# Kernel tuning notes

Hardware: AMD Instinct MI355X
Metric: run time of the kernel (lower is better)

Reference implementation:

```python
import jax, jax.numpy as jnp
import numpy as np

T, B, I = 512, 64, 768
H, L = 768, 2


def setup_inputs() -> dict:
    key = jax.random.key(0)
    ks = jax.random.split(key, 8)
    s = 1.0 / np.sqrt(H)
    return {
        "event_seq": jax.random.normal(ks[0], (T, B, I), jnp.float32),
        "h0": jax.random.normal(ks[1], (L, B, H), jnp.float32),
        "c0": jax.random.normal(ks[2], (L, B, H), jnp.float32),
        "W_ih": jax.random.uniform(ks[3], (L, 4 * H, I), jnp.float32, -s, s),
        "W_hh": jax.random.uniform(ks[4], (L, 4 * H, H), jnp.float32, -s, s),
        "b_ih": jax.random.uniform(ks[5], (L, 4 * H), jnp.float32, -s, s),
        "b_hh": jax.random.uniform(ks[6], (L, 4 * H), jnp.float32, -s, s),
        "length": jax.random.randint(ks[7], (B,), 1, T + 1, jnp.int32),
    }


def reference(event_seq, h0, c0, W_ih, W_hh, b_ih, b_hh, length):
    # event_seq: [T, B, I]; h0/c0: [L, B, H]; W_ih/W_hh: [L, 4H, *]
    ts = jnp.arange(event_seq.shape[0])

    def step(carry, xt_t):
        h, c = carry                      # [L, B, H] each
        x_t, t = xt_t
        mask = (t < length).astype(x_t.dtype)[:, None]  # [B, 1]
        x = x_t
        hs, cs = [], []
        for l in range(L):
            gates = x @ W_ih[l].T + b_ih[l] + h[l] @ W_hh[l].T + b_hh[l]
            i_g, f_g, g_g, o_g = jnp.split(gates, 4, axis=-1)  # torch LSTMCell order
            c_new = jax.nn.sigmoid(f_g) * c[l] + jax.nn.sigmoid(i_g) * jnp.tanh(g_g)
            h_new = jax.nn.sigmoid(o_g) * jnp.tanh(c_new)
            h_new = mask * h_new + (1.0 - mask) * h[l]
            c_new = mask * c_new + (1.0 - mask) * c[l]
            hs.append(h_new)
            cs.append(c_new)
            x = h_new  # dropout=0 -> identity between layers
        h = jnp.stack(hs)
        c = jnp.stack(cs)
        return (h, c), h

    (h_f, c_f), out = jax.lax.scan(step, (h0, c0), (event_seq, ts))
    # out: [T, L, B, H] -> [T, B, L, H] (matches torch.stack(..., dim=2))
    out = out.transpose(0, 2, 1, 3)
    return out, h_f, c_f
```

## Files before the change

### kernel.cpp

```cpp
#include <hip/hip_runtime.h>

typedef unsigned short u16;
typedef unsigned int u32;
typedef unsigned long long u64;
typedef __attribute__((ext_vector_type(8))) short short8;
typedef __attribute__((ext_vector_type(4))) float f32x4;

#define T_STEPS 512
#define HF_OFF 50331648UL
#define SLOT 49152

#define BCAT_OFF 18874368UL
#define HB0_OFF  18898944UL
#define HB1_OFF  (HB0_OFF + 32UL*98304UL)
#define FLG_OFF  (HB1_OFF + 4UL*98304UL)

__device__ __forceinline__ u16 f2bf(float f) {
  union { float f; unsigned u; } v; v.f = f;
  unsigned r = (v.u + 0x7FFFu + ((v.u >> 16) & 1u)) >> 16;
  return (u16)r;
}

__device__ __forceinline__ short8 pack8(float4 f0, float4 f1) {
  short8 v;
  v[0]=(short)f2bf(f0.x); v[1]=(short)f2bf(f0.y); v[2]=(short)f2bf(f0.z); v[3]=(short)f2bf(f0.w);
  v[4]=(short)f2bf(f1.x); v[5]=(short)f2bf(f1.y); v[6]=(short)f2bf(f1.z); v[7]=(short)f2bf(f1.w);
  return v;
}

__device__ __forceinline__ float sigm(float x) { return 1.0f / (1.0f + __expf(-x)); }
__device__ __forceinline__ float tanh_f(float x) { return 1.0f - 2.0f / (__expf(2.0f * x) + 1.0f); }

__device__ __forceinline__ short8 load_sc_b128(const void* p) {
  short8 r;
  asm volatile("global_load_dwordx4 %0, %1, off sc0 sc1" : "=&v"(r) : "v"((u64)p));
  return r;
}
__device__ __forceinline__ u32 load_sc_b32(const u32* p) {
  u32 r;
  asm volatile("global_load_dword %0, %1, off sc0 sc1\n\ts_waitcnt vmcnt(0)"
               : "=&v"(r) : "v"((u64)p) : "memory");
  return r;
}
__device__ __forceinline__ void store_sc_b32(u32* p, u32 v) {
  asm volatile("global_store_dword %0, %1, off sc0 sc1" :: "v"((u64)p), "v"(v) : "memory");
}

__device__ __forceinline__ void poll1(const u32* base, int own) {
  const int ln = threadIdx.x & 63;
  for (;;) {
    u32 f = load_sc_b32(base + ln);
    if (ln == own) f = 1u;
    if (__all(f != 0)) break;
    __builtin_amdgcn_s_sleep(1);
  }
}

__device__ __forceinline__ void stage_u16(u16* dstL, const u16* srcRow, int row, int uu) {
  short8 hv[6];
#pragma unroll
  for (int i = 0; i < 6; ++i) {
    int unit = uu + i * 16;
    int kel = (unit * 8) ^ ((row & 7) << 3);
    hv[i] = load_sc_b128(srcRow + kel);
  }
  __builtin_amdgcn_sched_barrier(0);
  asm volatile("s_waitcnt vmcnt(0)" ::: "memory");
  __builtin_amdgcn_sched_barrier(0);
#pragma unroll
  for (int i = 0; i < 6; ++i) {
    int unit = uu + i * 16;
    *(short8*)((char*)dstL + row * 1536 + unit * 16) = hv[i];
  }
}

__device__ __forceinline__ void stage_xf(u16* dstL, const float* srcRow, int row, int uu) {
#pragma unroll
  for (int i = 0; i < 6; ++i) {
    int unit = uu + i * 16;
    int kel = (unit * 8) ^ ((row & 7) << 3);
    float4 f0 = *(const float4*)(srcRow + kel);
    float4 f1 = *(const float4*)(srcRow + kel + 4);
    *(short8*)((char*)dstL + row * 1536 + unit * 16) = pack8(f0, f1);
  }
}

__global__ void prep_weights(const float* __restrict__ Wih, const float* __restrict__ Whh,
                             u16* __restrict__ Wr) {
  int idx = blockIdx.x * blockDim.x + threadIdx.x;
  if (idx >= 2 * 3072 * 192) return;
  int r = idx / 192;
  int kc = (idx - r * 192) * 8;
  int l = r / 3072;
  int rr = r - l * 3072;
  int j = rr >> 2, g = rr & 3;
  int srow = l * 3072 + g * 768 + j;
  const float* src = (kc < 768) ? (Wih + (size_t)srow * 768 + kc)
                                : (Whh + (size_t)srow * 768 + (kc - 768));
  float4 f0 = *(const float4*)src;
  float4 f1 = *(const float4*)(src + 4);
  *(short8*)(Wr + (size_t)r * 1536 + kc) = pack8(f0, f1);
}

__global__ void prep_misc(const float* __restrict__ h0, const float* __restrict__ bih,
                          const float* __restrict__ bhh, u16* __restrict__ hb0,
                          u16* __restrict__ hb1, float* __restrict__ bcat,
                          u32* __restrict__ flags) {
  int idx = blockIdx.x * blockDim.x + threadIdx.x;
  if (idx < 131584) {
    flags[idx] = (((idx >> 7) % 514) == 0) ? 1u : 0u;
  } else if (idx < 131584 + 98304) {
    int r = idx - 131584;
    int l = r / 49152, o = r - l * 49152;
    u16 v = f2bf(h0[r]);
    if (l == 0) hb0[o] = v; else hb1[o] = v;
  } else if (idx < 131584 + 98304 + 6144) {
    int q = idx - (131584 + 98304);
    int l = q / 3072, rr = q - l * 3072;
    int j = rr >> 2, g = rr & 3;
    int s = l * 3072 + g * 768 + j;
    bcat[q] = bih[s] + bhh[s];
  }
}

__global__ void __launch_bounds__(512, 1)
lstm_dataflow(const float* __restrict__ x, const float* __restrict__ h0,
              const float* __restrict__ c0, const int* __restrict__ len,
              const u16* __restrict__ Wr, const float* __restrict__ bcat,
              u16* __restrict__ hb0, u16* __restrict__ hb1,
              u32* __restrict__ flags, float* __restrict__ out) {
  __shared__ u16 lAh[32 * 768];
  __shared__ u16 lAx[32 * 768];
  __shared__ float pP[48 * 32 * 4];
  __shared__ u16 lH[32 * 12];

  const int tid = threadIdx.x;
  const int wv = tid >> 6;
  const int ln = tid & 63;
  const int ks = wv & 3;
  const int rt = wv >> 2;
  const int wg = blockIdx.x;
  const int layer = wg >> 7;
  const int rg = (wg >> 6) & 1;
  const int cg = wg & 63;
  const int n0 = cg * 48;
  const int row = tid >> 4;
  const int uu = tid & 15;
  const int arow = rt * 16 + (ln & 15);

  short8 Wx[3][6], Wh[3][6];
  {
    const u16* wbase = Wr + (size_t)(layer * 3072 + n0) * 1536;
#pragma unroll
    for (int ct = 0; ct < 3; ++ct)
#pragma unroll
      for (int kst = 0; kst < 6; ++kst) {
        int col = ct * 16 + (ln & 15);
        int k = ks * 192 + kst * 32 + ((ln >> 4) << 3);
        Wx[ct][kst] = *(const short8*)(wbase + (size_t)col * 1536 + k);
        Wh[ct][kst] = *(const short8*)(wbase + (size_t)col * 1536 + 768 + k);
      }
  }
  float bc[3] = {0.f, 0.f, 0.f};
  if (ks == 0) {
#pragma unroll
    for (int ct = 0; ct < 3; ++ct)
      bc[ct] = bcat[layer * 3072 + n0 + ct * 16 + (ln & 15)];
  }
  const int cellb = tid / 12, cellj = tid - (tid / 12) * 12;
  float cReg = 0.f, hKeep = 0.f; int lenB = 0;
  if (tid < 384) {
    int b = rg * 32 + cellb, j = cg * 12 + cellj;
    cReg = c0[(size_t)(layer * 64 + b) * 768 + j];
    hKeep = h0[(size_t)(layer * 64 + b) * 768 + j];
    lenB = len[b];
  }

  f32x4 acc_x[3];
  auto run_xmfma = [&]() {
#pragma unroll
    for (int ct = 0; ct < 3; ++ct)
      acc_x[ct] = (ks == 0) ? (f32x4){bc[ct], bc[ct], bc[ct], bc[ct]}
                            : (f32x4){0.f, 0.f, 0.f, 0.f};
#pragma unroll
    for (int kst = 0; kst < 6; ++kst) {
      int kel = ks * 192 + kst * 32 + ((ln >> 4) << 3);
      short8 a = *(const short8*)((const char*)lAx + arow * 1536 + ((kel * 2) ^ ((arow & 7) << 4)));
#pragma unroll
      for (int ct = 0; ct < 3; ++ct)
        acc_x[ct] = __builtin_amdgcn_mfma_f32_16x16x32_bf16(a, Wx[ct][kst], acc_x[ct], 0, 0, 0);
    }
  };
  auto stage_x = [&](int u) {
    if (layer == 0) {
      stage_xf(lAx, x + ((size_t)u * 64 + rg * 32 + row) * 768, row, uu);
    } else {
      poll1(flags + ((size_t)(0 * 514 + (u + 1)) * 2 + rg) * 64, -1);
      stage_u16(lAx, hb0 + (size_t)((u + 1) & 31) * SLOT + (size_t)(rg * 32 + row) * 768, row, uu);
    }
  };

  stage_x(0);
  __syncthreads();
  run_xmfma();
  __syncthreads();

  for (int t = 0; t < T_STEPS; ++t) {
    if (t < T_STEPS - 1) stage_x(t + 1);

    poll1(flags + ((size_t)(layer * 514 + t) * 2 + rg) * 64, cg);
    {
      const u16* hp = (layer == 0) ? hb0 + (size_t)(t & 31) * SLOT
                                   : hb1 + (size_t)(t & 3) * SLOT;
      stage_u16(lAh, hp + (size_t)(rg * 32 + row) * 768, row, uu);
    }
    __syncthreads();

    f32x4 acc[3];
#pragma unroll
    for (int ct = 0; ct < 3; ++ct) acc[ct] = acc_x[ct];
#pragma unroll
    for (int kst = 0; kst < 6; ++kst) {
      int kel = ks * 192 + kst * 32 + ((ln >> 4) << 3);
      short8 a = *(const short8*)((const char*)lAh + arow * 1536 + ((kel * 2) ^ ((arow & 7) << 4)));
#pragma unroll
      for (int ct = 0; ct < 3; ++ct)
        acc[ct] = __builtin_amdgcn_mfma_f32_16x16x32_bf16(a, Wh[ct][kst], acc[ct], 0, 0, 0);
    }

#pragma unroll
    for (int ct = 0; ct < 3; ++ct) {
      int col = ct * 16 + (ln & 15);
      int kwp = ks ^ (col & 3);
#pragma unroll
      for (int i = 0; i < 4; ++i) {
        int bloc = rt * 16 + ((ln >> 4) << 2) + i;
        pP[col * 128 + ((bloc ^ (col & 7)) << 2) + kwp] = acc[ct][i];
      }
    }
    __syncthreads();

    if (tid < 384) {
      float g4[4];
#pragma unroll
      for (int g = 0; g < 4; ++g) {
        int col = cellj * 4 + g;
        f32x4 v = *(const f32x4*)&pP[col * 128 + ((cellb ^ (col & 7)) << 2)];
        g4[g] = (v[0] + v[1]) + (v[2] + v[3]);
      }
      float cn = sigm(g4[1]) * cReg + sigm(g4[0]) * tanh_f(g4[2]);
      float hn = sigm(g4[3]) * tanh_f(cn);
      const bool act = t < lenB;
      float hm = act ? hn : hKeep;
      float cm = act ? cn : cReg;
      hKeep = hm; cReg = cm;
      const int bglob = rg * 32 + cellb, jglob = cg * 12 + cellj;
      lH[cellb * 12 + cellj] = f2bf(hm);
      out[((size_t)(t * 64 + bglob) * 2 + layer) * 768 + jglob] = hm;
    }
    __syncthreads();

    if (wv == 7) {
      u16* hout = (layer == 0) ? hb0 + (size_t)((t + 1) & 31) * SLOT
                               : hb1 + (size_t)((t + 1) & 3) * SLOT;
      const u32* lH32 = (const u32*)lH;
#pragma unroll
      for (int it = 0; it < 3; ++it) {
        int idx = ln + it * 64;
        int r = idx / 6, w = idx - (idx / 6) * 6;
        store_sc_b32((u32*)((char*)hout + (size_t)(rg * 32 + r) * 1536 + cg * 24 + w * 4),
                     lH32[r * 6 + w]);
      }
      asm volatile("s_waitcnt vmcnt(0)" ::: "memory");
      if (ln == 0)
        store_sc_b32(flags + ((size_t)(layer * 514 + (t + 1)) * 2 + rg) * 64 + cg, 1u);
    }
    if (t < T_STEPS - 1) run_xmfma();
    if (layer == 0 && (t & 7) == 0 && t >= 8)
      poll1(flags + ((size_t)(1 * 514 + (t - 8)) * 2 + rg) * 64, -1);
    __syncthreads();
  }

  if (tid < 384) {
    int b = rg * 32 + cellb, j = cg * 12 + cellj;
    float* hf = out + HF_OFF;
    float* cf = out + HF_OFF + 98304;
    hf[(size_t)(layer * 64 + b) * 768 + j] = hKeep;
    cf[(size_t)(layer * 64 + b) * 768 + j] = cReg;
  }
}

extern "C" void kernel_launch(void* const* d_in, const int* in_sizes, int n_in,
                              void* d_out, int out_size, void* d_ws, size_t ws_size,
                              hipStream_t stream) {
  const float* x   = (const float*)d_in[0];
  const float* h0  = (const float*)d_in[1];
  const float* c0  = (const float*)d_in[2];
  const float* Wih = (const float*)d_in[3];
  const float* Whh = (const float*)d_in[4];
  const float* bih = (const float*)d_in[5];
  const float* bhh = (const float*)d_in[6];
  const int*   len = (const int*)d_in[7];
  float* out = (float*)d_out;

  u16*   Wr    = (u16*)d_ws;
  float* bcat  = (float*)((char*)d_ws + BCAT_OFF);
  u16*   hb0   = (u16*)((char*)d_ws + HB0_OFF);
  u16*   hb1   = (u16*)((char*)d_ws + HB1_OFF);
  u32*   flags = (u32*)((char*)d_ws + FLG_OFF);

  {
    const int units = 2 * 3072 * 192;
    prep_weights<<<(units + 255) / 256, 256, 0, stream>>>(Wih, Whh, Wr);
    const int n2 = 131584 + 98304 + 6144;
    prep_misc<<<(n2 + 255) / 256, 256, 0, stream>>>(h0, bih, bhh, hb0, hb1, bcat, flags);
  }

  void* args[] = { (void*)&x, (void*)&h0, (void*)&c0, (void*)&len,
                   (void*)&Wr, (void*)&bcat, (void*)&hb0, (void*)&hb1,
                   (void*)&flags, (void*)&out };
  hipLaunchCooperativeKernel((const void*)lstm_dataflow, dim3(256), dim3(512),
                             args, 0, stream);
}
```

Measured before the change: 4.082 ms.

## Replace flag-based h handoff with per-element step-tagged words in hidden buffers

Each hidden-state element is now published as a 32-bit word that packs the bf16 value with a 16-bit timestep tag. Consumers poll the data itself until every tag matches, so the separate flag write, the flag poll and the LDS gather/extra barrier before publishing are removed. The cost is twice the hidden-buffer traffic, retry loops over 12 vector loads, and ring depth cut from 32 to 16 slots. Layer-1 progress flags are kept only for layer 0's back-pressure check, which now uses a shorter lag.

After: 6.109 ms. 1.5x slower.

```diff
diff --git a/kernel.cpp b/kernel.cpp
--- a/kernel.cpp
+++ b/kernel.cpp
@@ -5,15 +5,16 @@
 typedef unsigned long long u64;
 typedef __attribute__((ext_vector_type(8))) short short8;
 typedef __attribute__((ext_vector_type(4))) float f32x4;
+typedef __attribute__((ext_vector_type(4))) unsigned int u32x4;
 
 #define T_STEPS 512
 #define HF_OFF 50331648UL
-#define SLOT 49152
+#define HSLOT 49152UL
 
 #define BCAT_OFF 18874368UL
 #define HB0_OFF  18898944UL
-#define HB1_OFF  (HB0_OFF + 32UL*98304UL)
-#define FLG_OFF  (HB1_OFF + 4UL*98304UL)
+#define HB1_OFF  (HB0_OFF + 16UL*196608UL)
+#define FLG_OFF  (HB1_OFF + 4UL*196608UL)
 
 __device__ __forceinline__ u16 f2bf(float f) {
   union { float f; unsigned u; } v; v.f = f;
@@ -31,11 +32,6 @@
 __device__ __forceinline__ float sigm(float x) { return 1.0f / (1.0f + __expf(-x)); }
 __device__ __forceinline__ float tanh_f(float x) { return 1.0f - 2.0f / (__expf(2.0f * x) + 1.0f); }
 
-__device__ __forceinline__ short8 load_sc_b128(const void* p) {
-  short8 r;
-  asm volatile("global_load_dwordx4 %0, %1, off sc0 sc1" : "=&v"(r) : "v"((u64)p));
-  return r;
-}
 __device__ __forceinline__ u32 load_sc_b32(const u32* p) {
   u32 r;
   asm volatile("global_load_dword %0, %1, off sc0 sc1\n\ts_waitcnt vmcnt(0)"
@@ -56,21 +52,39 @@
   }
 }
 
-__device__ __forceinline__ void stage_u16(u16* dstL, const u16* srcRow, int row, int uu) {
-  short8 hv[6];
+__device__ __forceinline__ void stage_tagged(u16* dstL, const u32* src, int row, int uu, u32 tag) {
+  u32x4 v[12];
+  const int sw = (row & 7) << 3;
+  const u32* b2 = src + ((uu * 8) ^ sw);
+  u32 stale = 0xFFFu;
+  for (;;) {
+#pragma unroll
+    for (int q = 0; q < 12; ++q)
+      if (stale & (1u << q))
+        asm volatile("global_load_dwordx4 %0, %1, off sc0 sc1"
+                     : "=&v"(v[q]) : "v"((u64)(b2 + (q >> 1) * 128 + (q & 1) * 4)));
+    asm volatile("s_waitcnt vmcnt(0)" ::: "memory");
+    u32 ns = 0;
+#pragma unroll
+    for (int q = 0; q < 12; ++q)
+      if (stale & (1u << q)) {
+        if (((v[q][0] & 0xffffu) != tag) | ((v[q][1] & 0xffffu) != tag) |
+            ((v[q][2] & 0xffffu) != tag) | ((v[q][3] & 0xffffu) != tag))
+          ns |= 1u << q;
+      }
+    if (ns == 0) break;
+    stale = ns;
+    __builtin_amdgcn_s_sleep(1);
+  }
 #pragma unroll
   for (int i = 0; i < 6; ++i) {
     int unit = uu + i * 16;
-    int kel = (unit * 8) ^ ((row & 7) << 3);
-    hv[i] = load_sc_b128(srcRow + kel);
-  }
-  __builtin_amdgcn_sched_barrier(0);
-  asm volatile("s_waitcnt vmcnt(0)" ::: "memory");
-  __builtin_amdgcn_sched_barrier(0);
-#pragma unroll
-  for (int i = 0; i < 6; ++i) {
-    int unit = uu + i * 16;
-    *(short8*)((char*)dstL + row * 1536 + unit * 16) = hv[i];
+    u32x4 w;
+    w[0] = __builtin_amdgcn_perm(v[2*i][1],   v[2*i][0],   0x07060302u);
+    w[1] = __builtin_amdgcn_perm(v[2*i][3],   v[2*i][2],   0x07060302u);
+    w[2] = __builtin_amdgcn_perm(v[2*i+1][1], v[2*i+1][0], 0x07060302u);
+    w[3] = __builtin_amdgcn_perm(v[2*i+1][3], v[2*i+1][2], 0x07060302u);
+    *(u32x4*)((char*)dstL + row * 1536 + unit * 16) = w;
   }
 }
 
@@ -103,8 +117,8 @@
 }
 
 __global__ void prep_misc(const float* __restrict__ h0, const float* __restrict__ bih,
-                          const float* __restrict__ bhh, u16* __restrict__ hb0,
-                          u16* __restrict__ hb1, float* __restrict__ bcat,
+                          const float* __restrict__ bhh, u32* __restrict__ hb0,
+                          u32* __restrict__ hb1, float* __restrict__ bcat,
                           u32* __restrict__ flags) {
   int idx = blockIdx.x * blockDim.x + threadIdx.x;
   if (idx < 131584) {
@@ -112,7 +126,7 @@
   } else if (idx < 131584 + 98304) {
     int r = idx - 131584;
     int l = r / 49152, o = r - l * 49152;
-    u16 v = f2bf(h0[r]);
+    u32 v = ((u32)f2bf(h0[r]) << 16);
     if (l == 0) hb0[o] = v; else hb1[o] = v;
   } else if (idx < 131584 + 98304 + 6144) {
     int q = idx - (131584 + 98304);
@@ -127,12 +141,11 @@
 lstm_dataflow(const float* __restrict__ x, const float* __restrict__ h0,
               const float* __restrict__ c0, const int* __restrict__ len,
               const u16* __restrict__ Wr, const float* __restrict__ bcat,
-              u16* __restrict__ hb0, u16* __restrict__ hb1,
+              u32* __restrict__ hb0, u32* __restrict__ hb1,
               u32* __restrict__ flags, float* __restrict__ out) {
   __shared__ u16 lAh[32 * 768];
   __shared__ u16 lAx[32 * 768];
   __shared__ float pP[48 * 32 * 4];
-  __shared__ u16 lH[32 * 12];
 
   const int tid = threadIdx.x;
   const int wv = tid >> 6;
@@ -195,8 +208,8 @@
     if (layer == 0) {
       stage_xf(lAx, x + ((size_t)u * 64 + rg * 32 + row) * 768, row, uu);
     } else {
-      poll1(flags + ((size_t)(0 * 514 + (u + 1)) * 2 + rg) * 64, -1);
-      stage_u16(lAx, hb0 + (size_t)((u + 1) & 31) * SLOT + (size_t)(rg * 32 + row) * 768, row, uu);
+      stage_tagged(lAx, hb0 + (size_t)((u + 1) & 15) * HSLOT + (size_t)(rg * 32 + row) * 768,
+                   row, uu, (u32)(u + 1));
     }
   };
 
@@ -206,14 +219,13 @@
   __syncthreads();
 
   for (int t = 0; t < T_STEPS; ++t) {
+    {
+      const u32* hsrc = (layer == 0 ? hb0 + (size_t)(t & 15) * HSLOT
+                                    : hb1 + (size_t)(t & 3) * HSLOT)
+                        + (size_t)(rg * 32 + row) * 768;
+      stage_tagged(lAh, hsrc, row, uu, (u32)t);
+    }
     if (t < T_STEPS - 1) stage_x(t + 1);
-
-    poll1(flags + ((size_t)(layer * 514 + t) * 2 + rg) * 64, cg);
-    {
-      const u16* hp = (layer == 0) ? hb0 + (size_t)(t & 31) * SLOT
-                                   : hb1 + (size_t)(t & 3) * SLOT;
-      stage_u16(lAh, hp + (size_t)(rg * 32 + row) * 768, row, uu);
-    }
     __syncthreads();
 
     f32x4 acc[3];
@@ -255,29 +267,18 @@
       float cm = act ? cn : cReg;
       hKeep = hm; cReg = cm;
       const int bglob = rg * 32 + cellb, jglob = cg * 12 + cellj;
-      lH[cellb * 12 + cellj] = f2bf(hm);
+      u32* hpub = (layer == 0) ? hb0 + (size_t)((t + 1) & 15) * HSLOT
+                               : hb1 + (size_t)((t + 1) & 3) * HSLOT;
+      u32 word = ((u32)f2bf(hm) << 16) | ((u32)(t + 1) & 0xffffu);
+      store_sc_b32(hpub + (size_t)bglob * 768 + jglob, word);
       out[((size_t)(t * 64 + bglob) * 2 + layer) * 768 + jglob] = hm;
-    }
-    __syncthreads();
-
-    if (wv == 7) {
-      u16* hout = (layer == 0) ? hb0 + (size_t)((t + 1) & 31) * SLOT
-                               : hb1 + (size_t)((t + 1) & 3) * SLOT;
-      const u32* lH32 = (const u32*)lH;
-#pragma unroll
-      for (int it = 0; it < 3; ++it) {
-        int idx = ln + it * 64;
-        int r = idx / 6, w = idx - (idx / 6) * 6;
-        store_sc_b32((u32*)((char*)hout + (size_t)(rg * 32 + r) * 1536 + cg * 24 + w * 4),
-                     lH32[r * 6 + w]);
-      }
-      asm volatile("s_waitcnt vmcnt(0)" ::: "memory");
-      if (ln == 0)
-        store_sc_b32(flags + ((size_t)(layer * 514 + (t + 1)) * 2 + rg) * 64 + cg, 1u);
-    }
+      if (layer == 1 && tid == 0)
+        store_sc_b32(flags + ((size_t)(514 + (t + 1)) * 2 + rg) * 64 + cg, 1u);
+    }
+
     if (t < T_STEPS - 1) run_xmfma();
     if (layer == 0 && (t & 7) == 0 && t >= 8)
-      poll1(flags + ((size_t)(1 * 514 + (t - 8)) * 2 + rg) * 64, -1);
+      poll1(flags + ((size_t)(514 + (t - 4)) * 2 + rg) * 64, -1);
     __syncthreads();
   }
 
@@ -305,8 +306,8 @@
 
   u16*   Wr    = (u16*)d_ws;
   float* bcat  = (float*)((char*)d_ws + BCAT_OFF);
-  u16*   hb0   = (u16*)((char*)d_ws + HB0_OFF);
-  u16*   hb1   = (u16*)((char*)d_ws + HB1_OFF);
+  u32*   hb0   = (u32*)((char*)d_ws + HB0_OFF);
+  u32*   hb1   = (u32*)((char*)d_ws + HB1_OFF);
   u32*   flags = (u32*)((char*)d_ws + FLG_OFF);
 
   {
```

## Merge layer-1 flag polls and h/x staging loads, pad LDS rows

Applied to the files above, without the earlier changes.

For layer 1, the two separate waits (own-layer h flag and layer-0 output flag) become a single combined poll, and both 768-wide bf16 rows are fetched with interleaved coherent loads under one vmcnt wait. The goal is to cut one full polling and global-load round trip from the serial recurrence critical path. LDS rows are padded from 1536 to 1568 bytes to change the bank mapping, and the layer-0 hidden ring buffer shrinks from 32 to 16 slots. The risk is that layer 1 now waits on layer 0's step earlier in each iteration, and the smaller ring needs the existing throttling poll to stay ahead of slot reuse.

After: 5.105 ms. +25.1%, slower.

```diff
diff --git a/kernel.cpp b/kernel.cpp
--- a/kernel.cpp
+++ b/kernel.cpp
@@ -8,11 +8,12 @@
 
 #define T_STEPS 512
 #define HF_OFF 50331648UL
-#define SLOT 49152
+#define HSLOT 49152UL
+#define LROWB 1568
 
 #define BCAT_OFF 18874368UL
 #define HB0_OFF  18898944UL
-#define HB1_OFF  (HB0_OFF + 32UL*98304UL)
+#define HB1_OFF  (HB0_OFF + 16UL*98304UL)
 #define FLG_OFF  (HB1_OFF + 4UL*98304UL)
 
 __device__ __forceinline__ u16 f2bf(float f) {
@@ -56,6 +57,17 @@
   }
 }
 
+__device__ __forceinline__ void poll2(const u32* b0, int own0, const u32* b1) {
+  const int ln = threadIdx.x & 63;
+  for (;;) {
+    u32 f0 = load_sc_b32(b0 + ln);
+    u32 f1 = load_sc_b32(b1 + ln);
+    if (ln == own0) f0 = 1u;
+    if (__all((f0 != 0) && (f1 != 0))) break;
+    __builtin_amdgcn_s_sleep(1);
+  }
+}
+
 __device__ __forceinline__ void stage_u16(u16* dstL, const u16* srcRow, int row, int uu) {
   short8 hv[6];
 #pragma unroll
@@ -70,7 +82,7 @@
 #pragma unroll
   for (int i = 0; i < 6; ++i) {
     int unit = uu + i * 16;
-    *(short8*)((char*)dstL + row * 1536 + unit * 16) = hv[i];
+    *(short8*)((char*)dstL + row * LROWB + unit * 16) = hv[i];
   }
 }
 
@@ -81,7 +93,7 @@
     int kel = (unit * 8) ^ ((row & 7) << 3);
     float4 f0 = *(const float4*)(srcRow + kel);
     float4 f1 = *(const float4*)(srcRow + kel + 4);
-    *(short8*)((char*)dstL + row * 1536 + unit * 16) = pack8(f0, f1);
+    *(short8*)((char*)dstL + row * LROWB + unit * 16) = pack8(f0, f1);
   }
 }
 
@@ -129,8 +141,8 @@
               const u16* __restrict__ Wr, const float* __restrict__ bcat,
               u16* __restrict__ hb0, u16* __restrict__ hb1,
               u32* __restrict__ flags, float* __restrict__ out) {
-  __shared__ u16 lAh[32 * 768];
-  __shared__ u16 lAx[32 * 768];
+  __shared__ u16 lAh[32 * 784];
+  __shared__ u16 lAx[32 * 784];
   __shared__ float pP[48 * 32 * 4];
   __shared__ u16 lH[32 * 12];
 
@@ -185,34 +197,55 @@
 #pragma unroll
     for (int kst = 0; kst < 6; ++kst) {
       int kel = ks * 192 + kst * 32 + ((ln >> 4) << 3);
-      short8 a = *(const short8*)((const char*)lAx + arow * 1536 + ((kel * 2) ^ ((arow & 7) << 4)));
+      short8 a = *(const short8*)((const char*)lAx + arow * LROWB + ((kel * 2) ^ ((arow & 7) << 4)));
 #pragma unroll
       for (int ct = 0; ct < 3; ++ct)
         acc_x[ct] = __builtin_amdgcn_mfma_f32_16x16x32_bf16(a, Wx[ct][kst], acc_x[ct], 0, 0, 0);
     }
   };
-  auto stage_x = [&](int u) {
-    if (layer == 0) {
-      stage_xf(lAx, x + ((size_t)u * 64 + rg * 32 + row) * 768, row, uu);
-    } else {
-      poll1(flags + ((size_t)(0 * 514 + (u + 1)) * 2 + rg) * 64, -1);
-      stage_u16(lAx, hb0 + (size_t)((u + 1) & 31) * SLOT + (size_t)(rg * 32 + row) * 768, row, uu);
-    }
-  };
-
-  stage_x(0);
+
+  if (layer == 0) {
+    stage_xf(lAx, x + (size_t)(rg * 32 + row) * 768, row, uu);
+  } else {
+    poll1(flags + ((size_t)(0 * 514 + 1) * 2 + rg) * 64, -1);
+    stage_u16(lAx, hb0 + (size_t)1 * HSLOT + (size_t)(rg * 32 + row) * 768, row, uu);
+  }
   __syncthreads();
   run_xmfma();
   __syncthreads();
 
   for (int t = 0; t < T_STEPS; ++t) {
-    if (t < T_STEPS - 1) stage_x(t + 1);
-
-    poll1(flags + ((size_t)(layer * 514 + t) * 2 + rg) * 64, cg);
-    {
-      const u16* hp = (layer == 0) ? hb0 + (size_t)(t & 31) * SLOT
-                                   : hb1 + (size_t)(t & 3) * SLOT;
-      stage_u16(lAh, hp + (size_t)(rg * 32 + row) * 768, row, uu);
+    if (layer == 0) {
+      if (t < T_STEPS - 1)
+        stage_xf(lAx, x + ((size_t)(t + 1) * 64 + rg * 32 + row) * 768, row, uu);
+      poll1(flags + ((size_t)(0 * 514 + t) * 2 + rg) * 64, cg);
+      stage_u16(lAh, hb0 + (size_t)(t & 15) * HSLOT + (size_t)(rg * 32 + row) * 768, row, uu);
+    } else {
+      if (t < T_STEPS - 1) {
+        poll2(flags + ((size_t)(514 + t) * 2 + rg) * 64, cg,
+              flags + ((size_t)(0 * 514 + (t + 2)) * 2 + rg) * 64);
+        const u16* hp = hb1 + (size_t)(t & 3) * HSLOT + (size_t)(rg * 32 + row) * 768;
+        const u16* xp = hb0 + (size_t)((t + 2) & 15) * HSLOT + (size_t)(rg * 32 + row) * 768;
+        short8 hv[6], xv[6];
+#pragma unroll
+        for (int i = 0; i < 6; ++i) {
+          int kel = ((uu + i * 16) * 8) ^ ((row & 7) << 3);
+          hv[i] = load_sc_b128(hp + kel);
+          xv[i] = load_sc_b128(xp + kel);
+        }
+        __builtin_amdgcn_sched_barrier(0);
+        asm volatile("s_waitcnt vmcnt(0)" ::: "memory");
+        __builtin_amdgcn_sched_barrier(0);
+#pragma unroll
+        for (int i = 0; i < 6; ++i) {
+          int unit = uu + i * 16;
+          *(short8*)((char*)lAh + row * LROWB + unit * 16) = hv[i];
+          *(short8*)((char*)lAx + row * LROWB + unit * 16) = xv[i];
+        }
+      } else {
+        poll1(flags + ((size_t)(514 + t) * 2 + rg) * 64, cg);
+        stage_u16(lAh, hb1 + (size_t)(t & 3) * HSLOT + (size_t)(rg * 32 + row) * 768, row, uu);
+      }
     }
     __syncthreads();
 
@@ -222,7 +255,7 @@
 #pragma unroll
     for (int kst = 0; kst < 6; ++kst) {
       int kel = ks * 192 + kst * 32 + ((ln >> 4) << 3);
-      short8 a = *(const short8*)((const char*)lAh + arow * 1536 + ((kel * 2) ^ ((arow & 7) << 4)));
+      short8 a = *(const short8*)((const char*)lAh + arow * LROWB + ((kel * 2) ^ ((arow & 7) << 4)));
 #pragma unroll
       for (int ct = 0; ct < 3; ++ct)
         acc[ct] = __builtin_amdgcn_mfma_f32_16x16x32_bf16(a, Wh[ct][kst], acc[ct], 0, 0, 0);
@@ -261,8 +294,8 @@
     __syncthreads();
 
     if (wv == 7) {
-      u16* hout = (layer == 0) ? hb0 + (size_t)((t + 1) & 31) * SLOT
-                               : hb1 + (size_t)((t + 1) & 3) * SLOT;
+      u16* hout = (layer == 0) ? hb0 + (size_t)((t + 1) & 15) * HSLOT
+                               : hb1 + (size_t)((t + 1) & 3) * HSLOT;
       const u32* lH32 = (const u32*)lH;
 #pragma unroll
       for (int it = 0; it < 3; ++it) {
```
